# Kernel tuning notes

Hardware: AMD Instinct MI355X
Metric: run time of the kernel (lower is better)

Reference implementation:

```python
import jax, jax.numpy as jnp
import numpy as np

B, T, D = 16, 512, 256
HH = D // 2   # per-direction hidden of bidirectional GRU
G, Z, R, NA = 32, 8, 16, 18


def _gru_step(h, x, wih, whh, bih, bhh):
    # torch.nn.GRUCell math
    gi = x @ wih.T + bih
    gh = h @ whh.T + bhh
    ir, iz, inn = jnp.split(gi, 3, axis=-1)
    hr, hz, hn = jnp.split(gh, 3, axis=-1)
    r = jax.nn.sigmoid(ir + hr)
    z = jax.nn.sigmoid(iz + hz)
    n = jnp.tanh(inn + r * hn)
    return (1.0 - z) * n + z * h


def _gru_seq(x_tbd, wih, whh, bih, bhh):
    h0 = jnp.zeros((x_tbd.shape[1], whh.shape[1]), x_tbd.dtype)
    def step(h, x):
        h = _gru_step(h, x, wih, whh, bih, bhh)
        return h, h
    _, hs = jax.lax.scan(step, h0, x_tbd)
    return hs  # (T, B, H)


def setup_inputs() -> dict:
    key = jax.random.key(0)
    ks = jax.random.split(key, 26)
    rn = lambda k, s, sc: jax.random.normal(k, s, jnp.float32) * sc
    d = {
        'e_seq': rn(ks[0], (B, T, D), 1.0),
        'eps':   rn(ks[1], (B, T, Z), 1.0),
        # acausal bidirectional GRU (fwd + bwd cells)
        'wih_f': rn(ks[2], (3 * HH, D), D ** -0.5),  'whh_f': rn(ks[3], (3 * HH, HH), HH ** -0.5),
        'bih_f': jnp.zeros((3 * HH,)), 'bhh_f': jnp.zeros((3 * HH,)),
        'wih_b': rn(ks[4], (3 * HH, D), D ** -0.5),  'whh_b': rn(ks[5], (3 * HH, HH), HH ** -0.5),
        'bih_b': jnp.zeros((3 * HH,)), 'bhh_b': jnp.zeros((3 * HH,)),
        # controller encoder GRUCell(2D -> G) + heads
        'wih_e': rn(ks[6], (3 * G, 2 * D), (2 * D) ** -0.5), 'whh_e': rn(ks[7], (3 * G, G), G ** -0.5),
        'bih_e': jnp.zeros((3 * G,)), 'bhh_e': jnp.zeros((3 * G,)),
        'mu_w': rn(ks[8], (Z, G), G ** -0.5),  'mu_b': jnp.zeros((Z,)),
        'lv_w': rn(ks[9], (Z, G), G ** -0.5),  'lv_b': jnp.zeros((Z,)),
        # switching unit MLP (D+G+Z -> 64 -> 1)
        'sw1_w': rn(ks[10], (64, D + G + Z), (D + G + Z) ** -0.5), 'sw1_b': jnp.zeros((64,)),
        'sw2_w': rn(ks[11], (1, 64), 64 ** -0.5), 'sw2_b': jnp.zeros((1,)),
        # decoder hypernet (Z -> 32 -> 2*D*R)
        'dec1_w': rn(ks[12], (32, Z), Z ** -0.5), 'dec1_b': jnp.zeros((32,)),
        'dec2_w': rn(ks[13], (2 * D * R, 32), 32 ** -0.5), 'dec2_b': jnp.zeros((2 * D * R,)),
        # final norm + action head
        'ln_g': jnp.ones((D,)), 'ln_b': jnp.zeros((D,)),
        'head_w': rn(ks[14], (NA, D), D ** -0.5), 'head_b': jnp.zeros((NA,)),
    }
    return d


def _forward(e_seq, eps, wih_f, whh_f, bih_f, bhh_f, wih_b, whh_b, bih_b, bhh_b,
             wih_e, whh_e, bih_e, bhh_e, mu_w, mu_b, lv_w, lv_b,
             sw1_w, sw1_b, sw2_w, sw2_b, dec1_w, dec1_b, dec2_w, dec2_b,
             ln_g, ln_b, head_w, head_b):
    Bz, Tt, Dm = e_seq.shape
    e_tbd = jnp.swapaxes(e_seq, 0, 1)                      # (T, B, D)
    # AcausalEmbedder: bidirectional GRU
    fwd = _gru_seq(e_tbd, wih_f, whh_f, bih_f, bhh_f)
    bwd = _gru_seq(e_tbd[::-1], wih_b, whh_b, bih_b, bhh_b)[::-1]
    s_tbd = jnp.concatenate([fwd, bwd], axis=-1)           # (T, B, D)
    eps_tbd = jnp.swapaxes(eps, 0, 1)

    h0 = jnp.zeros((Bz, whh_e.shape[1]), e_seq.dtype)
    z0 = jnp.zeros((Bz, mu_w.shape[0]), e_seq.dtype)

    def step(carry, xs):
        h, z_prev = carry
        e_t, s_t, eps_t = xs
        h = _gru_step(h, jnp.concatenate([e_t, s_t], axis=-1), wih_e, whh_e, bih_e, bhh_e)
        mu = h @ mu_w.T + mu_b
        logvar = h @ lv_w.T + lv_b
        # switching unit uses updated h (causal)
        hid = jnp.tanh(jnp.concatenate([e_t, h, z_prev], axis=-1) @ sw1_w.T + sw1_b)
        beta = jax.nn.sigmoid(hid @ sw2_w.T + sw2_b)       # (B, 1)
        z = beta * (mu + jnp.exp(0.5 * logvar) * eps_t) + (1.0 - beta) * z_prev
        return (h, jax.lax.stop_gradient(z)), (mu, logvar, beta, z)

    _, (mu_t, lv_t, be_t, z_t) = jax.lax.scan(step, (h0, z0), (e_tbd, s_tbd, eps_tbd))
    mu_seq = jnp.swapaxes(mu_t, 0, 1)
    logvar_seq = jnp.swapaxes(lv_t, 0, 1)
    beta_seq = jnp.swapaxes(be_t, 0, 1)
    z_seq = jnp.swapaxes(z_t, 0, 1)                        # (B, T, Z)

    # ControllerDecoder: z -> (A, Bm); apply U = A @ Bm^T without materializing U
    hmid = jnp.tanh(z_seq @ dec1_w.T + dec1_b)
    ab = hmid @ dec2_w.T + dec2_b                          # (B, T, 2*D*R)
    DR = ab.shape[-1] // 2
    A = ab[..., :DR].reshape(Bz, Tt, Dm, -1)               # (B, T, D, R)
    Bm = ab[..., DR:].reshape(Bz, Tt, Dm, -1)
    tmp = jnp.einsum('btdr,btd->btr', Bm, e_seq)
    perturbed = e_seq + jnp.einsum('btdr,btr->btd', A, tmp)

    # final LayerNorm + action head on obs positions
    mean = perturbed.mean(-1, keepdims=True)
    var = perturbed.var(-1, keepdims=True)
    xn = (perturbed - mean) * jax.lax.rsqrt(var + 1e-5) * ln_g + ln_b
    logits = xn @ head_w.T + head_b                        # (B, T, NA)
    return logits, mu_seq, logvar_seq, beta_seq, z_seq


def reference(e_seq, eps, wih_f, whh_f, bih_f, bhh_f, wih_b, whh_b, bih_b, bhh_b,
              wih_e, whh_e, bih_e, bhh_e, mu_w, mu_b, lv_w, lv_b,
              sw1_w, sw1_b, sw2_w, sw2_b, dec1_w, dec1_b, dec2_w, dec2_b,
              ln_g, ln_b, head_w, head_b):
    return _forward(e_seq, eps, wih_f, whh_f, bih_f, bhh_f, wih_b, whh_b, bih_b, bhh_b,
                    wih_e, whh_e, bih_e, bhh_e, mu_w, mu_b, lv_w, lv_b,
                    sw1_w, sw1_b, sw2_w, sw2_b, dec1_w, dec1_b, dec2_w, dec2_b,
                    ln_g, ln_b, head_w, head_b)
```

## Files before the change

kernel.cpp:

```cpp
#include <hip/hip_runtime.h>

#define TT 512
#define BB 16
#define DD 256
#define HHH 128
#define GG 32
#define ZZ 8
#define RR_ 16
#define NAA 18

typedef _Float16 h2v __attribute__((ext_vector_type(2)));
typedef __attribute__((ext_vector_type(4))) float f4;
typedef __attribute__((ext_vector_type(4))) int i4;

__device__ __forceinline__ float sigmoid_(float x) { return 1.f / (1.f + __expf(-x)); }
__device__ __forceinline__ float tanh_(float x) { float e = __expf(2.f * x); return 1.f - 2.f / (e + 1.f); }
__device__ __forceinline__ float dot4(float4 a, float4 b) {
    return a.x * b.x + a.y * b.y + a.z * b.z + a.w * b.w;
}
__device__ __forceinline__ h2v u2h2(unsigned u) { union { unsigned u; h2v h; } c; c.u = u; return c.h; }

__device__ __forceinline__ void lds_barrier() {
    asm volatile("s_waitcnt lgkmcnt(0)" ::: "memory");
    __builtin_amdgcn_s_barrier();
}

template <int CTRL, int RM, int BM, bool BC>
__device__ __forceinline__ float dpp_add_f(float v) {
    return v + __int_as_float(__builtin_amdgcn_update_dpp(0, __float_as_int(v), CTRL, RM, BM, BC));
}
__device__ __forceinline__ float wave_sum_bcast(float p) {
    p = dpp_add_f<0x111, 0xf, 0xf, true>(p);
    p = dpp_add_f<0x112, 0xf, 0xf, true>(p);
    p = dpp_add_f<0x114, 0xf, 0xf, true>(p);
    p = dpp_add_f<0x118, 0xf, 0xf, true>(p);
    p = dpp_add_f<0x142, 0xa, 0xf, false>(p);
    p = dpp_add_f<0x143, 0xc, 0xf, false>(p);
    return __int_as_float(__builtin_amdgcn_readlane(__float_as_int(p), 63));
}
__device__ __forceinline__ float quad_sum(float v) {
    v = dpp_add_f<0xB1, 0xf, 0xf, true>(v);
    v = dpp_add_f<0x4E, 0xf, 0xf, true>(v);
    return v;
}
__device__ __forceinline__ float rdlane(float v, int l) {
    return __int_as_float(__builtin_amdgcn_readlane(__float_as_int(v), l));
}

__global__ __launch_bounds__(256) void pack_w(
    const float* __restrict__ wf, const float* __restrict__ wb,
    const float* __restrict__ we,
    unsigned* __restrict__ pk, unsigned* __restrict__ pk_e)
{
    int i = blockIdx.x * 256 + threadIdx.x;
    if (i < 49152) {
        int dir = i / 24576; int r = i % 24576;
        int w = r / 3072;    int r2 = r % 3072;
        int T = r2 / 1024;   int r3 = r2 % 1024;
        int kt = r3 / 256;   int r4 = r3 % 256;
        int lane = r4 / 4;   int jd = r4 % 4;
        const float* wsrc = dir ? wb : wf;
        int row = T * 128 + 16 * w + (lane & 15);
        int k0 = kt * 32 + (lane >> 4) * 8 + 2 * jd;
        union { _Float16 h[2]; unsigned u; } c;
        c.h[0] = (_Float16)wsrc[row * 128 + k0];
        c.h[1] = (_Float16)wsrc[row * 128 + k0 + 1];
        pk[i] = c.u;
    } else if (i < 50688) {
        int ie = i - 49152;
        int s = ie / 384;  int rem = ie % 384;
        int k = rem / 12;  int e = rem % 12;
        int j = e / 4;     int m = e % 4;
        int row = j * 32 + k, k0 = 8 * s + 2 * m;
        union { _Float16 h[2]; unsigned u; } c;
        c.h[0] = (_Float16)we[row * 32 + k0];
        c.h[1] = (_Float16)we[row * 32 + k0 + 1];
        pk_e[ie] = c.u;
    }
}

__global__ __launch_bounds__(256) void gemm_k(
    const float* __restrict__ A, int K, const float* __restrict__ W, int ldw,
    const float* __restrict__ bias, float* __restrict__ Out, int ldout, int N, int accFlag)
{
    __shared__ float At[64][36];
    __shared__ float Wt[32][36];
    int row0 = blockIdx.x * 64, n0 = blockIdx.y * 32;
    int tid = threadIdx.x;
    int tx = tid & 15, ty = tid >> 4;
    float acc[4][2] = {};
    for (int k0 = 0; k0 < K; k0 += 32) {
        #pragma unroll
        for (int i = 0; i < 8; ++i) {
            int idx = tid + i * 256; int rr = idx >> 5, kk = idx & 31;
            At[rr][kk] = A[(size_t)(row0 + rr) * K + k0 + kk];
        }
        #pragma unroll
        for (int i = 0; i < 4; ++i) {
            int idx = tid + i * 256; int nn = idx >> 5, kk = idx & 31;
            Wt[nn][kk] = (n0 + nn < N) ? W[(size_t)(n0 + nn) * ldw + k0 + kk] : 0.f;
        }
        __syncthreads();
        #pragma unroll
        for (int kk = 0; kk < 32; kk += 4) {
            float4 w0 = *(const float4*)&Wt[tx][kk];
            float4 w1 = *(const float4*)&Wt[tx + 16][kk];
            #pragma unroll
            for (int rr = 0; rr < 4; ++rr) {
                float4 av = *(const float4*)&At[ty * 4 + rr][kk];
                acc[rr][0] += dot4(av, w0);
                acc[rr][1] += dot4(av, w1);
            }
        }
        __syncthreads();
    }
    #pragma unroll
    for (int cc = 0; cc < 2; ++cc) {
        int n = n0 + tx + cc * 16;
        if (n < N) {
            float badd = bias ? bias[n] : 0.f;
            #pragma unroll
            for (int rr = 0; rr < 4; ++rr) {
                int row = row0 + ty * 4 + rr;
                float v = acc[rr][cc] + badd;
                if (accFlag) Out[(size_t)row * ldout + n] += v;
                else         Out[(size_t)row * ldout + n] = v;
            }
        }
    }
}

__global__ __launch_bounds__(256) void gemm_gi(
    const float* __restrict__ A,
    const float* __restrict__ wf, const float* __restrict__ bf, float* __restrict__ of,
    const float* __restrict__ wb, const float* __restrict__ bb, float* __restrict__ ob)
{
    __shared__ float At[64][36];
    __shared__ float Wt[32][36];
    int y = blockIdx.y;
    const float* W; const float* bias; float* Out; int n0;
    if (y < 12) { W = wf; bias = bf; Out = of; n0 = y * 32; }
    else        { W = wb; bias = bb; Out = ob; n0 = (y - 12) * 32; }
    int row0 = blockIdx.x * 64;
    int tid = threadIdx.x;
    int tx = tid & 15, ty = tid >> 4;
    float acc[4][2] = {};
    for (int k0 = 0; k0 < 256; k0 += 32) {
        #pragma unroll
        for (int i = 0; i < 8; ++i) {
            int idx = tid + i * 256; int rr = idx >> 5, kk = idx & 31;
            At[rr][kk] = A[(size_t)(row0 + rr) * 256 + k0 + kk];
        }
        #pragma unroll
        for (int i = 0; i < 4; ++i) {
            int idx = tid + i * 256; int nn = idx >> 5, kk = idx & 31;
            Wt[nn][kk] = W[(size_t)(n0 + nn) * 256 + k0 + kk];
        }
        __syncthreads();
        #pragma unroll
        for (int kk = 0; kk < 32; kk += 4) {
            float4 w0 = *(const float4*)&Wt[tx][kk];
            float4 w1 = *(const float4*)&Wt[tx + 16][kk];
            #pragma unroll
            for (int rr = 0; rr < 4; ++rr) {
                float4 av = *(const float4*)&At[ty * 4 + rr][kk];
                acc[rr][0] += dot4(av, w0);
                acc[rr][1] += dot4(av, w1);
            }
        }
        __syncthreads();
    }
    #pragma unroll
    for (int cc = 0; cc < 2; ++cc) {
        int n = n0 + tx + cc * 16;
        float badd = bias[n];
        #pragma unroll
        for (int rr = 0; rr < 4; ++rr) {
            int row = row0 + ty * 4 + rr;
            Out[(size_t)row * 384 + n] = acc[rr][cc] + badd;
        }
    }
}

struct __align__(16) SmGru { _Float16 hb[2][128]; };
struct __align__(16) SmGemm { float At[64][36]; float Wt[32][36]; };
union __align__(16) SmU { SmGru g; SmGemm m; };

__device__ __forceinline__ void gemm_tile512(
    const float* __restrict__ A, int K, const float* __restrict__ W, int ldw,
    const float* __restrict__ bias, float* __restrict__ Out, int ldout, int N,
    int row0, int n0, SmGemm& sm)
{
    int tid = threadIdx.x;
    int tx = tid & 31, ty = tid >> 5;
    float acc[4] = {};
    for (int k0 = 0; k0 < K; k0 += 32) {
        #pragma unroll
        for (int i = 0; i < 4; ++i) {
            int idx = tid + i * 512; int rr = idx >> 5, kk = idx & 31;
            sm.At[rr][kk] = A[(size_t)(row0 + rr) * K + k0 + kk];
        }
        #pragma unroll
        for (int i = 0; i < 2; ++i) {
            int idx = tid + i * 512; int nn = idx >> 5, kk = idx & 31;
            sm.Wt[nn][kk] = (n0 + nn < N) ? W[(size_t)(n0 + nn) * ldw + k0 + kk] : 0.f;
        }
        __syncthreads();
        #pragma unroll
        for (int kk = 0; kk < 32; kk += 4) {
            float4 w0 = *(const float4*)&sm.Wt[tx][kk];
            #pragma unroll
            for (int rr = 0; rr < 4; ++rr) {
                float4 av = *(const float4*)&sm.At[ty * 4 + rr][kk];
                acc[rr] += dot4(av, w0);
            }
        }
        __syncthreads();
    }
    int n = n0 + tx;
    if (n < N) {
        float badd = bias ? bias[n] : 0.f;
        #pragma unroll
        for (int rr = 0; rr < 4; ++rr)
            Out[(size_t)(row0 + ty * 4 + rr) * ldout + n] = acc[rr] + badd;
    }
}

__global__ __launch_bounds__(512, 2) void gru_fused(
    const float* __restrict__ gi_f, const float* __restrict__ gi_b,
    const unsigned* __restrict__ pk,
    const float* __restrict__ bhh_f, const float* __restrict__ bhh_b,
    float* __restrict__ s_seq,
    const float* __restrict__ e,
    const float* __restrict__ wih_e, const float* __restrict__ bih_e, float* __restrict__ gie,
    const float* __restrict__ sw1_w, const float* __restrict__ sw1_b, float* __restrict__ swe)
{
    __shared__ SmU sm;
    int bx = blockIdx.x;
    if (bx >= 416) {
        int t = bx - 416;
        gemm_tile512(e, 256, sw1_w, 296, sw1_b, swe, 64, 64, (t & 127) * 64, (t >> 7) * 32, sm.m);
        return;
    }
    if (bx >= 32) {
        int t = bx - 32;
        gemm_tile512(e, 256, wih_e, 512, bih_e, gie, 96, 96, (t & 127) * 64, (t >> 7) * 32, sm.m);
        return;
    }

    int dir = bx >> 4, b = bx & 15;
    const float* gi  = dir ? gi_b  : gi_f;
    const float* bhh = dir ? bhh_b : bhh_f;
    int tid = threadIdx.x;
    int w = tid >> 6;
    int lane = tid & 63;
    int quad = lane >> 4;
    int c = lane & 15;
    int j = 16 * w + c;

    i4 bf[3][4];
    #pragma unroll
    for (int T = 0; T < 3; ++T)
        #pragma unroll
        for (int kt = 0; kt < 4; ++kt)
            bf[T][kt] = *(const i4*)(pk + (size_t)((((dir * 8 + w) * 3 + T) * 4 + kt) * 64 + lane) * 4);
    #pragma unroll
    for (int T = 0; T < 3; ++T)
        #pragma unroll
        for (int kt = 0; kt < 4; ++kt)
            asm volatile("" : "+a"(bf[T][kt]));

    if (tid < 128) sm.g.hb[0][tid] = (_Float16)0.f;

    float bhr = 0.f, bhz = 0.f, bhn = 0.f;
    float gra = 0.f, gza = 0.f, gna = 0.f;
    float grb = 0.f, gzb = 0.f, gnb = 0.f;
    float hreg = 0.f;
    if (lane < 16) {
        bhr = bhh[j]; bhz = bhh[128 + j]; bhn = bhh[256 + j];
        int t0 = dir ? 511 : 0;
        int t1 = dir ? 510 : 1;
        size_t p0 = (size_t)(b * TT + t0) * 384;
        size_t p1 = (size_t)(b * TT + t1) * 384;
        gra = gi[p0 + j]; gza = gi[p0 + 128 + j]; gna = gi[p0 + 256 + j];
        grb = gi[p1 + j]; gzb = gi[p1 + 128 + j]; gnb = gi[p1 + 256 + j];
    }
    __syncthreads();

    int cur = 0;
    auto body = [&](int step, float& gr, float& gz, float& gn) {
        i4 af[4];
        #pragma unroll
        for (int kt = 0; kt < 4; ++kt)
            af[kt] = *(const i4*)(&sm.g.hb[cur][kt * 32 + quad * 8]);
        f4 accrA = {0.f, 0.f, 0.f, 0.f}, accrB = {0.f, 0.f, 0.f, 0.f};
        f4 acczA = {0.f, 0.f, 0.f, 0.f}, acczB = {0.f, 0.f, 0.f, 0.f};
        f4 accnA = {0.f, 0.f, 0.f, 0.f}, accnB = {0.f, 0.f, 0.f, 0.f};
        asm volatile("s_nop 3");
        asm volatile("v_mfma_f32_16x16x32_f16 %0, %1, %2, %0" : "+v"(accrA) : "v"(af[0]), "a"(bf[0][0]));
        asm volatile("v_mfma_f32_16x16x32_f16 %0, %1, %2, %0" : "+v"(acczA) : "v"(af[0]), "a"(bf[1][0]));
        asm volatile("v_mfma_f32_16x16x32_f16 %0, %1, %2, %0" : "+v"(accnA) : "v"(af[0]), "a"(bf[2][0]));
        asm volatile("v_mfma_f32_16x16x32_f16 %0, %1, %2, %0" : "+v"(accrB) : "v"(af[2]), "a"(bf[0][2]));
        asm volatile("v_mfma_f32_16x16x32_f16 %0, %1, %2, %0" : "+v"(acczB) : "v"(af[2]), "a"(bf[1][2]));
        asm volatile("v_mfma_f32_16x16x32_f16 %0, %1, %2, %0" : "+v"(accnB) : "v"(af[2]), "a"(bf[2][2]));
        asm volatile("v_mfma_f32_16x16x32_f16 %0, %1, %2, %0" : "+v"(accrA) : "v"(af[1]), "a"(bf[0][1]));
        asm volatile("v_mfma_f32_16x16x32_f16 %0, %1, %2, %0" : "+v"(acczA) : "v"(af[1]), "a"(bf[1][1]));
        asm volatile("v_mfma_f32_16x16x32_f16 %0, %1, %2, %0" : "+v"(accnA) : "v"(af[1]), "a"(bf[2][1]));
        asm volatile("v_mfma_f32_16x16x32_f16 %0, %1, %2, %0" : "+v"(accrB) : "v"(af[3]), "a"(bf[0][3]));
        asm volatile("v_mfma_f32_16x16x32_f16 %0, %1, %2, %0" : "+v"(acczB) : "v"(af[3]), "a"(bf[1][3]));
        asm volatile("v_mfma_f32_16x16x32_f16 %0, %1, %2, %0" : "+v"(accnB) : "v"(af[3]), "a"(bf[2][3]));
        asm volatile("s_nop 7\n\ts_nop 7");
        if (lane < 16) {
            int t = dir ? (511 - step) : step;
            int p = b * TT + t;
            float ar = accrA[0] + accrB[0];
            float az = acczA[0] + acczB[0];
            float an = accnA[0] + accnB[0];
            float r = sigmoid_(gr + bhr + ar);
            float z = sigmoid_(gz + bhz + az);
            float n = tanh_(gn + r * (bhn + an));
            float hn = (1.f - z) * n + z * hreg;
            hreg = hn;
            sm.g.hb[cur ^ 1][j] = (_Float16)hn;
            s_seq[(size_t)p * 256 + dir * 128 + j] = hn;
            int s2 = step + 2;
            int tp = (s2 < 512) ? (dir ? (511 - s2) : s2) : t;
            size_t p2 = (size_t)(b * TT + tp) * 384;
            gr = gi[p2 + j]; gz = gi[p2 + 128 + j]; gn = gi[p2 + 256 + j];
        }
        lds_barrier();
        cur ^= 1;
    };

    for (int step = 0; step < 512; step += 2) {
        body(step,     gra, gza, gna);
        body(step + 1, grb, gzb, gnb);
    }
}

__global__ __launch_bounds__(128, 1) void ctrl_fused(
    const float* __restrict__ gie, const unsigned* __restrict__ pk_e,
    const float* __restrict__ bhh_e,
    const float* __restrict__ mu_w, const float* __restrict__ mu_b,
    const float* __restrict__ lv_w, const float* __restrict__ lv_b,
    const float* __restrict__ sw1_w, const float* __restrict__ sw2_w,
    const float* __restrict__ sw2_b,
    const float* __restrict__ swe,
    const float* __restrict__ eps,
    float* __restrict__ out_mu, float* __restrict__ out_lv,
    float* __restrict__ beta_o, float* __restrict__ z_o)
{
    int b = blockIdx.x;
    int tid = threadIdx.x;
    int wid = tid >> 6;
    int lane = tid & 63;
    int pbase = b * TT;

    __shared__ __align__(16) _Float16 hb[8][32];
    __shared__ __align__(16) float    hf[8][32];

    int k = lane >> 1, s2 = lane & 1;
    unsigned wg[24];
    float bhr = 0.f, bhz = 0.f, bhn = 0.f, hreg = 0.f;
    float g1[4] = {}, g2[4] = {}, g3[4] = {};
    if (wid == 0) {
        #pragma unroll
        for (int ss = 0; ss < 2; ++ss) {
            const uint4* wp = (const uint4*)(pk_e + ((size_t)((2 * s2 + ss) * 32) + k) * 12);
            #pragma unroll
            for (int i = 0; i < 3; ++i) {
                uint4 u = wp[i];
                wg[12 * ss + 4 * i + 0] = u.x;
                wg[12 * ss + 4 * i + 1] = u.y;
                wg[12 * ss + 4 * i + 2] = u.z;
                wg[12 * ss + 4 * i + 3] = u.w;
            }
        }
        if (lane < 32) hb[7][lane] = (_Float16)0.f;
        if (s2 == 0) {
            bhr = bhh_e[k]; bhz = bhh_e[32 + k]; bhn = bhh_e[64 + k];
            #pragma unroll
            for (int i = 0; i < 4; ++i) {
                size_t p = (size_t)(pbase + i) * 96;
                g1[i] = gie[p + k]; g2[i] = gie[p + 32 + k]; g3[i] = gie[p + 64 + k];
            }
        }
    }

    int x = lane >> 3, kind = (lane >> 2) & 1, s = lane & 3;
    float4 swh4[8];
    float4 wz0v = {0,0,0,0}, wz1v = {0,0,0,0}, mlw0 = {0,0,0,0}, mlw1 = {0,0,0,0};
    float w2 = 0.f, sb2 = 0.f, mlb = 0.f;
    float4 zr0 = {0.f, 0.f, 0.f, 0.f}, zr1 = {0.f, 0.f, 0.f, 0.f};
    float hp[4] = {}, ep[4] = {};
    if (wid == 1) {
        #pragma unroll
        for (int i = 0; i < 8; ++i)
            swh4[i] = *(const float4*)(sw1_w + (size_t)lane * 296 + 256 + 4 * i);
        wz0v = *(const float4*)(sw1_w + (size_t)lane * 296 + 288);
        wz1v = *(const float4*)(sw1_w + (size_t)lane * 296 + 292);
        w2 = sw2_w[lane];
        sb2 = sw2_b[0];
        const float* mw = kind ? lv_w : mu_w;
        mlw0 = *(const float4*)(mw + x * 32 + 8 * s);
        mlw1 = *(const float4*)(mw + x * 32 + 8 * s + 4);
        mlb = kind ? lv_b[x] : mu_b[x];
        #pragma unroll
        for (int i = 0; i < 4; ++i) {
            hp[i] = swe[(size_t)(pbase + i) * 64 + lane];
            ep[i] = eps[(size_t)(pbase + i) * 8 + x];
        }
    }
    __syncthreads();

    auto prod_step = [&](int t, float& ga, float& gb, float& gc) {
        const uint4* hv = (const uint4*)(&hb[(t - 1) & 7][16 * s2]);
        uint4 hA = hv[0], hB = hv[1];
        unsigned hw[8] = {hA.x, hA.y, hA.z, hA.w, hB.x, hB.y, hB.z, hB.w};
        float a0 = 0.f, a1 = 0.f, a2 = 0.f, c0 = 0.f, c1 = 0.f, c2 = 0.f;
        #pragma unroll
        for (int m = 0; m < 4; ++m) {
            a0 = __builtin_amdgcn_fdot2(u2h2(wg[m]),      u2h2(hw[m]),     a0, false);
            a1 = __builtin_amdgcn_fdot2(u2h2(wg[4 + m]),  u2h2(hw[m]),     a1, false);
            a2 = __builtin_amdgcn_fdot2(u2h2(wg[8 + m]),  u2h2(hw[m]),     a2, false);
            c0 = __builtin_amdgcn_fdot2(u2h2(wg[12 + m]), u2h2(hw[4 + m]), c0, false);
            c1 = __builtin_amdgcn_fdot2(u2h2(wg[16 + m]), u2h2(hw[4 + m]), c1, false);
            c2 = __builtin_amdgcn_fdot2(u2h2(wg[20 + m]), u2h2(hw[4 + m]), c2, false);
        }
        a0 += c0; a1 += c1; a2 += c2;
        a0 = dpp_add_f<0xB1, 0xf, 0xf, true>(a0);
        a1 = dpp_add_f<0xB1, 0xf, 0xf, true>(a1);
        a2 = dpp_add_f<0xB1, 0xf, 0xf, true>(a2);
        if (s2 == 0) {
            float r = sigmoid_(ga + bhr + a0);
            float z = sigmoid_(gb + bhz + a1);
            float n = tanh_(gc + r * (bhn + a2));
            float hn = (1.f - z) * n + z * hreg;
            hreg = hn;
            hb[t & 7][k] = (_Float16)hn;
            hf[t & 7][k] = hn;
            int t4 = (t + 4 < 512) ? (t + 4) : t;
            size_t p2 = (size_t)(pbase + t4) * 96;
            ga = gie[p2 + k]; gb = gie[p2 + 32 + k]; gc = gie[p2 + 64 + k];
        }
    };

    auto cons_step = [&](int t, float& hpi, float& epi) {
        int sl = t & 7;
        const float4* hv4 = (const float4*)(&hf[sl][0]);
        float4 h0 = hv4[0], h1 = hv4[1], h2 = hv4[2], h3 = hv4[3];
        float4 h4 = hv4[4], h5 = hv4[5], h6 = hv4[6], h7 = hv4[7];
        float d0 = dot4(swh4[0], h0) + dot4(swh4[1], h1);
        float d1 = dot4(swh4[2], h2) + dot4(swh4[3], h3);
        float d2 = dot4(swh4[4], h4) + dot4(swh4[5], h5);
        float d3 = dot4(swh4[6], h6) + dot4(swh4[7], h7);
        float hsum = (d0 + d1) + (d2 + d3);
        float4 hs0 = *(const float4*)(&hf[sl][8 * s]);
        float4 hs1 = *(const float4*)(&hf[sl][8 * s + 4]);
        float pacc = quad_sum(dot4(mlw0, hs0) + dot4(mlw1, hs1));
        float v = pacc + mlb;
        float other = __int_as_float(__builtin_amdgcn_ds_swizzle(__float_as_int(v), 0x101F));
        float muv = kind ? other : v;
        float lvv = kind ? v : other;
        float cand = muv + __expf(0.5f * lvv) * epi;
        float sc0 = rdlane(cand, 0),  sc1 = rdlane(cand, 8);
        float sc2 = rdlane(cand, 16), sc3 = rdlane(cand, 24);
        float sc4 = rdlane(cand, 32), sc5 = rdlane(cand, 40);
        float sc6 = rdlane(cand, 48), sc7 = rdlane(cand, 56);
        float az = dot4(wz0v, zr0) + dot4(wz1v, zr1);
        float a = (hpi + hsum) + az;
        float hid = tanh_(a);
        float beta = sigmoid_(wave_sum_bcast(w2 * hid) + sb2);
        float omb = 1.f - beta;
        zr0.x = beta * sc0 + omb * zr0.x; zr0.y = beta * sc1 + omb * zr0.y;
        zr0.z = beta * sc2 + omb * zr0.z; zr0.w = beta * sc3 + omb * zr0.w;
        zr1.x = beta * sc4 + omb * zr1.x; zr1.y = beta * sc5 + omb * zr1.y;
        zr1.z = beta * sc6 + omb * zr1.z; zr1.w = beta * sc7 + omb * zr1.w;
        int p = pbase + t;
        if (lane == 0) {
            beta_o[p] = beta;
            *(float4*)(z_o + (size_t)p * 8)     = zr0;
            *(float4*)(z_o + (size_t)p * 8 + 4) = zr1;
        }
        if ((lane & 7) == 0) out_mu[(size_t)p * 8 + x] = muv;
        if ((lane & 7) == 4) out_lv[(size_t)p * 8 + x] = lvv;
        int t4 = (t + 4 < 512) ? (t + 4) : t;
        hpi = swe[(size_t)(pbase + t4) * 64 + lane];
        epi = eps[(size_t)(pbase + t4) * 8 + x];
    };

    for (int ph = 0; ph < 129; ++ph) {
        if (wid == 0) {
            if (ph < 128) {
                int t0 = ph * 4;
                prod_step(t0,     g1[0], g2[0], g3[0]);
                prod_step(t0 + 1, g1[1], g2[1], g3[1]);
                prod_step(t0 + 2, g1[2], g2[2], g3[2]);
                prod_step(t0 + 3, g1[3], g2[3], g3[3]);
            }
        } else {
            if (ph >= 1) {
                int t0 = (ph - 1) * 4;
                cons_step(t0,     hp[0], ep[0]);
                cons_step(t0 + 1, hp[1], ep[1]);
                cons_step(t0 + 2, hp[2], ep[2]);
                cons_step(t0 + 3, hp[3], ep[3]);
            }
        }
        lds_barrier();
    }
}

__global__ __launch_bounds__(256, 3) void decoder_final(
    const float* __restrict__ e_seq, const float* __restrict__ z_o,
    const float* __restrict__ dec1_w, const float* __restrict__ dec1_b,
    const float* __restrict__ dec2_w, const float* __restrict__ dec2_b,
    const float* __restrict__ ln_g, const float* __restrict__ ln_b,
    const float* __restrict__ head_w, const float* __restrict__ head_b,
    float* __restrict__ logits)
{
    __shared__ __align__(16) float e_l[8][256];
    __shared__ __align__(16) float hmid[8][32];
    __shared__ float zl[8][8];
    __shared__ float tmpw[8][16];
    __shared__ __align__(16) float partb[2048];
    __shared__ float red1[8][16];
    __shared__ float red2[8][16];
    __shared__ float stats[8][2];
    int tid = threadIdx.x;
    int p0 = blockIdx.x * 8;

    {
        const float4* eg = (const float4*)(e_seq + (size_t)p0 * 256);
        float4* el4 = (float4*)&e_l[0][0];
        el4[tid] = eg[tid];
        el4[tid + 256] = eg[tid + 256];
        if (tid < 64) ((float*)zl)[tid] = z_o[p0 * 8 + tid];
    }
    __syncthreads();
    {
        int pp = tid >> 5, g = tid & 31;
        float a = dec1_b[g];
        #pragma unroll
        for (int x = 0; x < 8; ++x) a += dec1_w[g * 8 + x] * zl[pp][x];
        hmid[pp][g] = tanh_(a);
    }
    __syncthreads();
    {
        int r = tid & 15, dgrp = tid >> 4;
        float acc[8];
        #pragma unroll
        for (int pp = 0; pp < 8; ++pp) acc[pp] = 0.f;
        for (int iblk = 0; iblk < 8; ++iblk) {
            float4 wr[2][8]; float wb[2]; int dd[2];
            #pragma unroll
            for (int ii = 0; ii < 2; ++ii) {
                int d = dgrp + 16 * (iblk * 2 + ii);
                dd[ii] = d;
                int row = 4096 + d * 16 + r;
                const float4* wp = (const float4*)(dec2_w + (size_t)row * 32);
                #pragma unroll
                for (int g = 0; g < 8; ++g) wr[ii][g] = wp[g];
                wb[ii] = dec2_b[row];
            }
            #pragma unroll 1
            for (int pp = 0; pp < 8; ++pp) {
                const float4* hv = (const float4*)hmid[pp];
                float b0 = wb[0], b1 = wb[1];
                #pragma unroll
                for (int g = 0; g < 8; ++g) {
                    float4 hh = hv[g];
                    b0 += dot4(wr[0][g], hh);
                    b1 += dot4(wr[1][g], hh);
                }
                acc[pp] += b0 * e_l[pp][dd[0]] + b1 * e_l[pp][dd[1]];
            }
        }
        #pragma unroll
        for (int pp = 0; pp < 8; ++pp) partb[(pp * 16 + r) * 16 + dgrp] = acc[pp];
    }
    __syncthreads();
    if (tid < 128) {
        int pp = tid >> 4, rr = tid & 15;
        float s = 0.f;
        #pragma unroll
        for (int dg = 0; dg < 16; ++dg) s += partb[(pp * 16 + rr) * 16 + dg];
        tmpw[pp][rr] = s;
    }
    __syncthreads();
    {
        int d = tid;
        float po[8];
        #pragma unroll
        for (int pp = 0; pp < 8; ++pp) po[pp] = e_l[pp][d];
        for (int rblk = 0; rblk < 8; ++rblk) {
            float4 wr[2][8]; float wb[2];
            #pragma unroll
            for (int ii = 0; ii < 2; ++ii) {
                int row = d * 16 + rblk * 2 + ii;
                const float4* wp = (const float4*)(dec2_w + (size_t)row * 32);
                #pragma unroll
                for (int g = 0; g < 8; ++g) wr[ii][g] = wp[g];
                wb[ii] = dec2_b[row];
            }
            #pragma unroll 1
            for (int pp = 0; pp < 8; ++pp) {
                const float4* hv = (const float4*)hmid[pp];
                float a0 = wb[0], a1 = wb[1];
                #pragma unroll
                for (int g = 0; g < 8; ++g) {
                    float4 hh = hv[g];
                    a0 += dot4(wr[0][g], hh);
                    a1 += dot4(wr[1][g], hh);
                }
                po[pp] += a0 * tmpw[pp][rblk * 2] + a1 * tmpw[pp][rblk * 2 + 1];
            }
        }
        #pragma unroll
        for (int pp = 0; pp < 8; ++pp) partb[pp * 256 + d] = po[pp];
    }
    __syncthreads();
    if (tid < 128) {
        int pp = tid >> 4, c = tid & 15;
        float s = 0.f, s2 = 0.f;
        #pragma unroll
        for (int i = 0; i < 16; ++i) { float v = partb[pp * 256 + c * 16 + i]; s += v; s2 += v * v; }
        red1[pp][c] = s; red2[pp][c] = s2;
    }
    __syncthreads();
    if (tid < 8) {
        float s = 0.f, s2 = 0.f;
        #pragma unroll
        for (int c = 0; c < 16; ++c) { s += red1[tid][c]; s2 += red2[tid][c]; }
        float mean = s * (1.f / 256.f);
        float var = s2 * (1.f / 256.f) - mean * mean;
        stats[tid][0] = mean;
        stats[tid][1] = rsqrtf(var + 1e-5f);
    }
    __syncthreads();
    {
        int d = tid;
        float g = ln_g[d], bln = ln_b[d];
        #pragma unroll
        for (int pp = 0; pp < 8; ++pp) {
            float v = (partb[pp * 256 + d] - stats[pp][0]) * stats[pp][1];
            partb[pp * 256 + d] = v * g + bln;
        }
    }
    __syncthreads();
    if (tid < 144) {
        int pp = tid / 18, na = tid - pp * 18;
        float a = head_b[na];
        for (int d2 = 0; d2 < 256; ++d2)
            a += partb[pp * 256 + d2] * head_w[na * 256 + d2];
        logits[(size_t)(p0 + pp) * 18 + na] = a;
    }
}

extern "C" void kernel_launch(void* const* d_in, const int* in_sizes, int n_in,
                              void* d_out, int out_size, void* d_ws, size_t ws_size,
                              hipStream_t stream) {
    (void)in_sizes; (void)n_in; (void)out_size; (void)ws_size;
    const float* e     = (const float*)d_in[0];
    const float* eps   = (const float*)d_in[1];
    const float* wih_f = (const float*)d_in[2];
    const float* whh_f = (const float*)d_in[3];
    const float* bih_f = (const float*)d_in[4];
    const float* bhh_f = (const float*)d_in[5];
    const float* wih_b = (const float*)d_in[6];
    const float* whh_b = (const float*)d_in[7];
    const float* bih_b = (const float*)d_in[8];
    const float* bhh_b = (const float*)d_in[9];
    const float* wih_e = (const float*)d_in[10];
    const float* whh_e = (const float*)d_in[11];
    const float* bih_e = (const float*)d_in[12];
    const float* bhh_e = (const float*)d_in[13];
    const float* mu_w  = (const float*)d_in[14];
    const float* mu_b  = (const float*)d_in[15];
    const float* lv_w  = (const float*)d_in[16];
    const float* lv_b  = (const float*)d_in[17];
    const float* sw1_w = (const float*)d_in[18];
    const float* sw1_b = (const float*)d_in[19];
    const float* sw2_w = (const float*)d_in[20];
    const float* sw2_b = (const float*)d_in[21];
    const float* dec1_w = (const float*)d_in[22];
    const float* dec1_b = (const float*)d_in[23];
    const float* dec2_w = (const float*)d_in[24];
    const float* dec2_b = (const float*)d_in[25];
    const float* ln_g  = (const float*)d_in[26];
    const float* ln_b  = (const float*)d_in[27];
    const float* head_w = (const float*)d_in[28];
    const float* head_b = (const float*)d_in[29];

    float* ws    = (float*)d_ws;
    float* gi_f  = ws;
    float* gi_b  = gi_f + 3145728;
    float* gie   = gi_b + 3145728;
    float* swe   = gie + 786432;
    float* s_seq = swe + 524288;
    float* h_seq = s_seq + 2097152;
    unsigned* pk   = (unsigned*)(h_seq + 262144);
    unsigned* pk_e = pk + 49152;
    (void)h_seq;

    float* out       = (float*)d_out;
    float* out_logit = out;
    float* out_mu    = out + 147456;
    float* out_lv    = out + 212992;
    float* out_beta  = out + 278528;
    float* out_z     = out + 286720;

    pack_w<<<198, 256, 0, stream>>>(whh_f, whh_b, whh_e, pk, pk_e);
    gemm_gi<<<dim3(128, 24), 256, 0, stream>>>(e, wih_f, bih_f, gi_f, wih_b, bih_b, gi_b);
    gru_fused<<<672, 512, 0, stream>>>(gi_f, gi_b, pk, bhh_f, bhh_b, s_seq,
                                       e, wih_e, bih_e, gie, sw1_w, sw1_b, swe);
    gemm_k<<<dim3(128, 3), 256, 0, stream>>>(s_seq, 256, wih_e + 256, 512, nullptr, gie, 96, 96, 1);
    ctrl_fused<<<16, 128, 0, stream>>>(gie, pk_e, bhh_e, mu_w, mu_b, lv_w, lv_b,
                                       sw1_w, sw2_w, sw2_b, swe, eps,
                                       out_mu, out_lv, out_beta, out_z);
    decoder_final<<<1024, 256, 0, stream>>>(e, out_z, dec1_w, dec1_b, dec2_w, dec2_b,
                                            ln_g, ln_b, head_w, head_b, out_logit);
}
```

Measured before the change: 918.5 us.

## Batch all 16 sequences per GRU direction into one block's MFMA rows

The recurrent GRU kernel previously ran one block per (direction, batch), using only one row of each 16x16 MFMA tile. Each direction now runs in a single block, with all 16 batch elements mapped to the MFMA M dimension, so every MFMA output row is useful. This cuts the recurrent blocks from 32 to 2. The hidden-state LDS buffer gets a padded layout (stride 17) to avoid bank conflicts, and each lane now handles 4 batch rows of gate math. The trade-off is more serial per-step work in each block and less parallelism across the GPU, since both directions now sit on only two CUs.

```diff
diff --git a/kernel.cpp b/kernel.cpp
--- a/kernel.cpp
+++ b/kernel.cpp
@@ -182,7 +182,8 @@
     }
 }
 
-struct __align__(16) SmGru { _Float16 hb[2][128]; };
+#define HB_ELEMS 2312
+struct __align__(16) SmGru { _Float16 hb[2][HB_ELEMS]; };
 struct __align__(16) SmGemm { float At[64][36]; float Wt[32][36]; };
 union __align__(16) SmU { SmGru g; SmGemm m; };
 
@@ -237,18 +238,18 @@
 {
     __shared__ SmU sm;
     int bx = blockIdx.x;
-    if (bx >= 416) {
-        int t = bx - 416;
+    if (bx >= 386) {
+        int t = bx - 386;
         gemm_tile512(e, 256, sw1_w, 296, sw1_b, swe, 64, 64, (t & 127) * 64, (t >> 7) * 32, sm.m);
         return;
     }
-    if (bx >= 32) {
-        int t = bx - 32;
+    if (bx >= 2) {
+        int t = bx - 2;
         gemm_tile512(e, 256, wih_e, 512, bih_e, gie, 96, 96, (t & 127) * 64, (t >> 7) * 32, sm.m);
         return;
     }
 
-    int dir = bx >> 4, b = bx & 15;
+    int dir = bx;
     const float* gi  = dir ? gi_b  : gi_f;
     const float* bhh = dir ? bhh_b : bhh_f;
     int tid = threadIdx.x;
@@ -257,6 +258,7 @@
     int quad = lane >> 4;
     int c = lane & 15;
     int j = 16 * w + c;
+    int kbj = j >> 3, jlo = j & 7;
 
     i4 bf[3][4];
     #pragma unroll
@@ -270,71 +272,69 @@
         for (int kt = 0; kt < 4; ++kt)
             asm volatile("" : "+a"(bf[T][kt]));
 
-    if (tid < 128) sm.g.hb[0][tid] = (_Float16)0.f;
-
-    float bhr = 0.f, bhz = 0.f, bhn = 0.f;
-    float gra = 0.f, gza = 0.f, gna = 0.f;
-    float grb = 0.f, gzb = 0.f, gnb = 0.f;
-    float hreg = 0.f;
-    if (lane < 16) {
-        bhr = bhh[j]; bhz = bhh[128 + j]; bhn = bhh[256 + j];
+    for (int i = tid; i < HB_ELEMS; i += 512) sm.g.hb[0][i] = (_Float16)0.f;
+
+    float bhr = bhh[j], bhz = bhh[128 + j], bhn = bhh[256 + j];
+    float hreg[4] = {0.f, 0.f, 0.f, 0.f};
+    size_t rb[4];
+    #pragma unroll
+    for (int reg = 0; reg < 4; ++reg)
+        rb[reg] = (size_t)(quad * 4 + reg) * TT * 384 + j;
+
+    float gA[4][3], gB[4][3];
+    {
         int t0 = dir ? 511 : 0;
         int t1 = dir ? 510 : 1;
-        size_t p0 = (size_t)(b * TT + t0) * 384;
-        size_t p1 = (size_t)(b * TT + t1) * 384;
-        gra = gi[p0 + j]; gza = gi[p0 + 128 + j]; gna = gi[p0 + 256 + j];
-        grb = gi[p1 + j]; gzb = gi[p1 + 128 + j]; gnb = gi[p1 + 256 + j];
+        #pragma unroll
+        for (int reg = 0; reg < 4; ++reg) {
+            size_t p0 = rb[reg] + (size_t)t0 * 384;
+            size_t p1 = rb[reg] + (size_t)t1 * 384;
+            gA[reg][0] = gi[p0]; gA[reg][1] = gi[p0 + 128]; gA[reg][2] = gi[p0 + 256];
+            gB[reg][0] = gi[p1]; gB[reg][1] = gi[p1 + 128]; gB[reg][2] = gi[p1 + 256];
+        }
     }
     __syncthreads();
 
     int cur = 0;
-    auto body = [&](int step, float& gr, float& gz, float& gn) {
+    auto body = [&](int step, float (&g)[4][3]) {
         i4 af[4];
         #pragma unroll
         for (int kt = 0; kt < 4; ++kt)
-            af[kt] = *(const i4*)(&sm.g.hb[cur][kt * 32 + quad * 8]);
-        f4 accrA = {0.f, 0.f, 0.f, 0.f}, accrB = {0.f, 0.f, 0.f, 0.f};
-        f4 acczA = {0.f, 0.f, 0.f, 0.f}, acczB = {0.f, 0.f, 0.f, 0.f};
-        f4 accnA = {0.f, 0.f, 0.f, 0.f}, accnB = {0.f, 0.f, 0.f, 0.f};
-        asm volatile("s_nop 3");
-        asm volatile("v_mfma_f32_16x16x32_f16 %0, %1, %2, %0" : "+v"(accrA) : "v"(af[0]), "a"(bf[0][0]));
-        asm volatile("v_mfma_f32_16x16x32_f16 %0, %1, %2, %0" : "+v"(acczA) : "v"(af[0]), "a"(bf[1][0]));
-        asm volatile("v_mfma_f32_16x16x32_f16 %0, %1, %2, %0" : "+v"(accnA) : "v"(af[0]), "a"(bf[2][0]));
-        asm volatile("v_mfma_f32_16x16x32_f16 %0, %1, %2, %0" : "+v"(accrB) : "v"(af[2]), "a"(bf[0][2]));
-        asm volatile("v_mfma_f32_16x16x32_f16 %0, %1, %2, %0" : "+v"(acczB) : "v"(af[2]), "a"(bf[1][2]));
-        asm volatile("v_mfma_f32_16x16x32_f16 %0, %1, %2, %0" : "+v"(accnB) : "v"(af[2]), "a"(bf[2][2]));
-        asm volatile("v_mfma_f32_16x16x32_f16 %0, %1, %2, %0" : "+v"(accrA) : "v"(af[1]), "a"(bf[0][1]));
-        asm volatile("v_mfma_f32_16x16x32_f16 %0, %1, %2, %0" : "+v"(acczA) : "v"(af[1]), "a"(bf[1][1]));
-        asm volatile("v_mfma_f32_16x16x32_f16 %0, %1, %2, %0" : "+v"(accnA) : "v"(af[1]), "a"(bf[2][1]));
-        asm volatile("v_mfma_f32_16x16x32_f16 %0, %1, %2, %0" : "+v"(accrB) : "v"(af[3]), "a"(bf[0][3]));
-        asm volatile("v_mfma_f32_16x16x32_f16 %0, %1, %2, %0" : "+v"(acczB) : "v"(af[3]), "a"(bf[1][3]));
-        asm volatile("v_mfma_f32_16x16x32_f16 %0, %1, %2, %0" : "+v"(accnB) : "v"(af[3]), "a"(bf[2][3]));
-        asm volatile("s_nop 7\n\ts_nop 7");
-        if (lane < 16) {
-            int t = dir ? (511 - step) : step;
-            int p = b * TT + t;
-            float ar = accrA[0] + accrB[0];
-            float az = acczA[0] + acczB[0];
-            float an = accnA[0] + accnB[0];
-            float r = sigmoid_(gr + bhr + ar);
-            float z = sigmoid_(gz + bhz + az);
-            float n = tanh_(gn + r * (bhn + an));
-            float hn = (1.f - z) * n + z * hreg;
-            hreg = hn;
-            sm.g.hb[cur ^ 1][j] = (_Float16)hn;
-            s_seq[(size_t)p * 256 + dir * 128 + j] = hn;
-            int s2 = step + 2;
-            int tp = (s2 < 512) ? (dir ? (511 - s2) : s2) : t;
-            size_t p2 = (size_t)(b * TT + tp) * 384;
-            gr = gi[p2 + j]; gz = gi[p2 + 128 + j]; gn = gi[p2 + 256 + j];
+            af[kt] = *(const i4*)(&sm.g.hb[cur][((kt * 4 + quad) * 17 + c) * 8]);
+        f4 accr = {0.f, 0.f, 0.f, 0.f};
+        f4 accz = {0.f, 0.f, 0.f, 0.f};
+        f4 accn = {0.f, 0.f, 0.f, 0.f};
+        asm volatile("s_nop 4" : "+v"(accr), "+v"(accz), "+v"(accn));
+        #pragma unroll
+        for (int kt = 0; kt < 4; ++kt) {
+            asm volatile("v_mfma_f32_16x16x32_f16 %0, %1, %2, %0" : "+v"(accr) : "v"(af[kt]), "a"(bf[0][kt]));
+            asm volatile("v_mfma_f32_16x16x32_f16 %0, %1, %2, %0" : "+v"(accz) : "v"(af[kt]), "a"(bf[1][kt]));
+            asm volatile("v_mfma_f32_16x16x32_f16 %0, %1, %2, %0" : "+v"(accn) : "v"(af[kt]), "a"(bf[2][kt]));
+        }
+        asm volatile("s_nop 7\n\ts_nop 7\n\ts_nop 7" : "+v"(accr), "+v"(accz), "+v"(accn));
+        int t = dir ? (511 - step) : step;
+        int sp = step + 2;
+        int tp = (sp < 512) ? (dir ? (511 - sp) : sp) : t;
+        #pragma unroll
+        for (int reg = 0; reg < 4; ++reg) {
+            int bt = quad * 4 + reg;
+            float r = sigmoid_(g[reg][0] + bhr + accr[reg]);
+            float z = sigmoid_(g[reg][1] + bhz + accz[reg]);
+            float n = tanh_(g[reg][2] + r * (bhn + accn[reg]));
+            float hn = (1.f - z) * n + z * hreg[reg];
+            hreg[reg] = hn;
+            s_seq[(size_t)(bt * TT + t) * 256 + dir * 128 + j] = hn;
+            sm.g.hb[cur ^ 1][(kbj * 17 + bt) * 8 + jlo] = (_Float16)hn;
+            size_t p2 = rb[reg] + (size_t)tp * 384;
+            g[reg][0] = gi[p2]; g[reg][1] = gi[p2 + 128]; g[reg][2] = gi[p2 + 256];
         }
         lds_barrier();
         cur ^= 1;
     };
 
     for (int step = 0; step < 512; step += 2) {
-        body(step,     gra, gza, gna);
-        body(step + 1, grb, gzb, gnb);
+        body(step,     gA);
+        body(step + 1, gB);
     }
 }
 
@@ -712,7 +712,7 @@
 
     pack_w<<<198, 256, 0, stream>>>(whh_f, whh_b, whh_e, pk, pk_e);
     gemm_gi<<<dim3(128, 24), 256, 0, stream>>>(e, wih_f, bih_f, gi_f, wih_b, bih_b, gi_b);
-    gru_fused<<<672, 512, 0, stream>>>(gi_f, gi_b, pk, bhh_f, bhh_b, s_seq,
+    gru_fused<<<642, 512, 0, stream>>>(gi_f, gi_b, pk, bhh_f, bhh_b, s_seq,
                                        e, wih_e, bih_e, gie, sw1_w, sw1_b, swe);
     gemm_k<<<dim3(128, 3), 256, 0, stream>>>(s_seq, 256, wih_e + 256, 512, nullptr, gie, 96, 96, 1);
     ctrl_fused<<<16, 128, 0, stream>>>(gie, pk_e, bhh_e, mu_w, mu_b, lv_w, lv_b,
```

After: 1.206 ms. 31.3% more time.

## Double controller pipeline chunk to 8 steps and serialize GRU MFMA accumulation

Applied to the files above, without the earlier changes.

The controller kernel's producer/consumer pipeline now processes 8 timesteps per phase instead of 4. The LDS history ring buffers and the register prefetch depth grow to match, which halves the number of block barriers. The bidirectional GRU step now uses three accumulators chained through all four k-tiles instead of six split A/B accumulators summed afterward. This removes the final adds but creates longer dependent MFMA chains, adding latency on the serial critical path.

```diff
diff --git a/kernel.cpp b/kernel.cpp
--- a/kernel.cpp
+++ b/kernel.cpp
@@ -293,32 +293,23 @@
         #pragma unroll
         for (int kt = 0; kt < 4; ++kt)
             af[kt] = *(const i4*)(&sm.g.hb[cur][kt * 32 + quad * 8]);
-        f4 accrA = {0.f, 0.f, 0.f, 0.f}, accrB = {0.f, 0.f, 0.f, 0.f};
-        f4 acczA = {0.f, 0.f, 0.f, 0.f}, acczB = {0.f, 0.f, 0.f, 0.f};
-        f4 accnA = {0.f, 0.f, 0.f, 0.f}, accnB = {0.f, 0.f, 0.f, 0.f};
-        asm volatile("s_nop 3");
-        asm volatile("v_mfma_f32_16x16x32_f16 %0, %1, %2, %0" : "+v"(accrA) : "v"(af[0]), "a"(bf[0][0]));
-        asm volatile("v_mfma_f32_16x16x32_f16 %0, %1, %2, %0" : "+v"(acczA) : "v"(af[0]), "a"(bf[1][0]));
-        asm volatile("v_mfma_f32_16x16x32_f16 %0, %1, %2, %0" : "+v"(accnA) : "v"(af[0]), "a"(bf[2][0]));
-        asm volatile("v_mfma_f32_16x16x32_f16 %0, %1, %2, %0" : "+v"(accrB) : "v"(af[2]), "a"(bf[0][2]));
-        asm volatile("v_mfma_f32_16x16x32_f16 %0, %1, %2, %0" : "+v"(acczB) : "v"(af[2]), "a"(bf[1][2]));
-        asm volatile("v_mfma_f32_16x16x32_f16 %0, %1, %2, %0" : "+v"(accnB) : "v"(af[2]), "a"(bf[2][2]));
-        asm volatile("v_mfma_f32_16x16x32_f16 %0, %1, %2, %0" : "+v"(accrA) : "v"(af[1]), "a"(bf[0][1]));
-        asm volatile("v_mfma_f32_16x16x32_f16 %0, %1, %2, %0" : "+v"(acczA) : "v"(af[1]), "a"(bf[1][1]));
-        asm volatile("v_mfma_f32_16x16x32_f16 %0, %1, %2, %0" : "+v"(accnA) : "v"(af[1]), "a"(bf[2][1]));
-        asm volatile("v_mfma_f32_16x16x32_f16 %0, %1, %2, %0" : "+v"(accrB) : "v"(af[3]), "a"(bf[0][3]));
-        asm volatile("v_mfma_f32_16x16x32_f16 %0, %1, %2, %0" : "+v"(acczB) : "v"(af[3]), "a"(bf[1][3]));
-        asm volatile("v_mfma_f32_16x16x32_f16 %0, %1, %2, %0" : "+v"(accnB) : "v"(af[3]), "a"(bf[2][3]));
-        asm volatile("s_nop 7\n\ts_nop 7");
+        f4 accr = {0.f, 0.f, 0.f, 0.f};
+        f4 accz = {0.f, 0.f, 0.f, 0.f};
+        f4 accn = {0.f, 0.f, 0.f, 0.f};
+        asm volatile("s_nop 3" : "+v"(accr), "+v"(accz), "+v"(accn));
+        #pragma unroll
+        for (int kt = 0; kt < 4; ++kt) {
+            asm volatile("v_mfma_f32_16x16x32_f16 %0, %1, %2, %0" : "+v"(accr) : "v"(af[kt]), "a"(bf[0][kt]));
+            asm volatile("v_mfma_f32_16x16x32_f16 %0, %1, %2, %0" : "+v"(accz) : "v"(af[kt]), "a"(bf[1][kt]));
+            asm volatile("v_mfma_f32_16x16x32_f16 %0, %1, %2, %0" : "+v"(accn) : "v"(af[kt]), "a"(bf[2][kt]));
+        }
+        asm volatile("s_nop 7\n\ts_nop 7" : "+v"(accr), "+v"(accz), "+v"(accn));
         if (lane < 16) {
             int t = dir ? (511 - step) : step;
             int p = b * TT + t;
-            float ar = accrA[0] + accrB[0];
-            float az = acczA[0] + acczB[0];
-            float an = accnA[0] + accnB[0];
-            float r = sigmoid_(gr + bhr + ar);
-            float z = sigmoid_(gz + bhz + az);
-            float n = tanh_(gn + r * (bhn + an));
+            float r = sigmoid_(gr + bhr + accr[0]);
+            float z = sigmoid_(gz + bhz + accz[0]);
+            float n = tanh_(gn + r * (bhn + accn[0]));
             float hn = (1.f - z) * n + z * hreg;
             hreg = hn;
             sm.g.hb[cur ^ 1][j] = (_Float16)hn;
@@ -356,13 +347,13 @@
     int lane = tid & 63;
     int pbase = b * TT;
 
-    __shared__ __align__(16) _Float16 hb[8][32];
-    __shared__ __align__(16) float    hf[8][32];
+    __shared__ __align__(16) _Float16 hb[16][32];
+    __shared__ __align__(16) float    hf[16][32];
 
     int k = lane >> 1, s2 = lane & 1;
     unsigned wg[24];
     float bhr = 0.f, bhz = 0.f, bhn = 0.f, hreg = 0.f;
-    float g1[4] = {}, g2[4] = {}, g3[4] = {};
+    float g1[8] = {}, g2[8] = {}, g3[8] = {};
     if (wid == 0) {
         #pragma unroll
         for (int ss = 0; ss < 2; ++ss) {
@@ -376,11 +367,11 @@
                 wg[12 * ss + 4 * i + 3] = u.w;
             }
         }
-        if (lane < 32) hb[7][lane] = (_Float16)0.f;
+        if (lane < 32) hb[15][lane] = (_Float16)0.f;
         if (s2 == 0) {
             bhr = bhh_e[k]; bhz = bhh_e[32 + k]; bhn = bhh_e[64 + k];
             #pragma unroll
-            for (int i = 0; i < 4; ++i) {
+            for (int i = 0; i < 8; ++i) {
                 size_t p = (size_t)(pbase + i) * 96;
                 g1[i] = gie[p + k]; g2[i] = gie[p + 32 + k]; g3[i] = gie[p + 64 + k];
             }
@@ -392,7 +383,7 @@
     float4 wz0v = {0,0,0,0}, wz1v = {0,0,0,0}, mlw0 = {0,0,0,0}, mlw1 = {0,0,0,0};
     float w2 = 0.f, sb2 = 0.f, mlb = 0.f;
     float4 zr0 = {0.f, 0.f, 0.f, 0.f}, zr1 = {0.f, 0.f, 0.f, 0.f};
-    float hp[4] = {}, ep[4] = {};
+    float hp[8] = {}, ep[8] = {};
     if (wid == 1) {
         #pragma unroll
         for (int i = 0; i < 8; ++i)
@@ -406,7 +397,7 @@
         mlw1 = *(const float4*)(mw + x * 32 + 8 * s + 4);
         mlb = kind ? lv_b[x] : mu_b[x];
         #pragma unroll
-        for (int i = 0; i < 4; ++i) {
+        for (int i = 0; i < 8; ++i) {
             hp[i] = swe[(size_t)(pbase + i) * 64 + lane];
             ep[i] = eps[(size_t)(pbase + i) * 8 + x];
         }
@@ -414,7 +405,7 @@
     __syncthreads();
 
     auto prod_step = [&](int t, float& ga, float& gb, float& gc) {
-        const uint4* hv = (const uint4*)(&hb[(t - 1) & 7][16 * s2]);
+        const uint4* hv = (const uint4*)(&hb[(t - 1) & 15][16 * s2]);
         uint4 hA = hv[0], hB = hv[1];
         unsigned hw[8] = {hA.x, hA.y, hA.z, hA.w, hB.x, hB.y, hB.z, hB.w};
         float a0 = 0.f, a1 = 0.f, a2 = 0.f, c0 = 0.f, c1 = 0.f, c2 = 0.f;
@@ -437,16 +428,16 @@
             float n = tanh_(gc + r * (bhn + a2));
             float hn = (1.f - z) * n + z * hreg;
             hreg = hn;
-            hb[t & 7][k] = (_Float16)hn;
-            hf[t & 7][k] = hn;
-            int t4 = (t + 4 < 512) ? (t + 4) : t;
-            size_t p2 = (size_t)(pbase + t4) * 96;
+            hb[t & 15][k] = (_Float16)hn;
+            hf[t & 15][k] = hn;
+            int t8 = (t + 8 < 512) ? (t + 8) : t;
+            size_t p2 = (size_t)(pbase + t8) * 96;
             ga = gie[p2 + k]; gb = gie[p2 + 32 + k]; gc = gie[p2 + 64 + k];
         }
     };
 
     auto cons_step = [&](int t, float& hpi, float& epi) {
-        int sl = t & 7;
+        int sl = t & 15;
         const float4* hv4 = (const float4*)(&hf[sl][0]);
         float4 h0 = hv4[0], h1 = hv4[1], h2 = hv4[2], h3 = hv4[3];
         float4 h4 = hv4[4], h5 = hv4[5], h6 = hv4[6], h7 = hv4[7];
@@ -484,27 +475,25 @@
         }
         if ((lane & 7) == 0) out_mu[(size_t)p * 8 + x] = muv;
         if ((lane & 7) == 4) out_lv[(size_t)p * 8 + x] = lvv;
-        int t4 = (t + 4 < 512) ? (t + 4) : t;
-        hpi = swe[(size_t)(pbase + t4) * 64 + lane];
-        epi = eps[(size_t)(pbase + t4) * 8 + x];
+        int t8 = (t + 8 < 512) ? (t + 8) : t;
+        hpi = swe[(size_t)(pbase + t8) * 64 + lane];
+        epi = eps[(size_t)(pbase + t8) * 8 + x];
     };
 
-    for (int ph = 0; ph < 129; ++ph) {
+    for (int ph = 0; ph < 65; ++ph) {
         if (wid == 0) {
-            if (ph < 128) {
-                int t0 = ph * 4;
-                prod_step(t0,     g1[0], g2[0], g3[0]);
-                prod_step(t0 + 1, g1[1], g2[1], g3[1]);
-                prod_step(t0 + 2, g1[2], g2[2], g3[2]);
-                prod_step(t0 + 3, g1[3], g2[3], g3[3]);
+            if (ph < 64) {
+                int t0 = ph * 8;
+                #pragma unroll
+                for (int i = 0; i < 8; ++i)
+                    prod_step(t0 + i, g1[i], g2[i], g3[i]);
             }
         } else {
             if (ph >= 1) {
-                int t0 = (ph - 1) * 4;
-                cons_step(t0,     hp[0], ep[0]);
-                cons_step(t0 + 1, hp[1], ep[1]);
-                cons_step(t0 + 2, hp[2], ep[2]);
-                cons_step(t0 + 3, hp[3], ep[3]);
+                int t0 = (ph - 1) * 8;
+                #pragma unroll
+                for (int i = 0; i < 8; ++i)
+                    cons_step(t0 + i, hp[i], ep[i]);
             }
         }
         lds_barrier();
```

Measured after the change: 898.3 us. 2.2% less time.
